# Kernel optimization log

Measured on AMD Instinct MI355X. Metric: run time of the kernel, lower is better.

## Reference

```python
import jax, jax.numpy as jnp
import numpy as np

B, V, D = 2048, 3129, 768  # batch, answer vocab, BERT embed dim


def setup_inputs() -> dict:
    key = jax.random.key(0)
    k1, k2, k3, k4 = jax.random.split(key, 4)
    prediction = jax.random.normal(k1, (B, V), dtype=jnp.float32)
    # sparse multi-label soft scores: ~10 nonzero answers per row (VQA-style)
    soft = jax.random.uniform(k2, (B, V), dtype=jnp.float32)
    keep = jax.random.uniform(k3, (B, V)) < 0.003
    label = jnp.where(keep, soft, 0.0)
    Embedding = jax.random.normal(k4, (V, D), dtype=jnp.float32)
    return {"prediction": prediction, "label": label, "Embedding": Embedding}


def reference(prediction, label, Embedding):
    V_ = Embedding.shape[0]
    # cosine-style normalization of the Gram matrix (row norms of sim itself,
    # exactly as in the torch code)
    sim = Embedding @ Embedding.T                              # [V, V]
    n = jnp.sqrt((sim ** 2).sum(1, keepdims=True))             # [V, 1]
    sim = sim / (n @ n.T + 1e-8)
    sim = jnp.where(jnp.eye(V_, dtype=bool), -2.0, sim)        # mask diagonal
    mapping = jnp.argmax(sim, axis=1)                          # [V] int

    # vectorized replacement of the per-batch/per-nonzero python loop:
    # semantic_a[i, mapping[g]] = label[i, g] for every nonzero label[i, g].
    # entries with label==0 are routed to out-of-bounds index V and dropped.
    Bn = label.shape[0]
    idx = jnp.where(label != 0, mapping[None, :], V_)          # [B, V]
    rows = jnp.arange(Bn)[:, None]                             # [B, 1]
    semantic_a = jnp.zeros_like(label).at[rows, idx].set(label, mode="drop")

    # BCE-with-logits, mean reduction, scaled by labels.size(1)
    bce = jnp.logaddexp(0.0, prediction) - prediction * semantic_a
    return jnp.mean(bce) * V_
```

## Files before the change

### kernel.cpp

```cpp
#include <hip/hip_runtime.h>
#include <hip/hip_bf16.h>

#define VN 3129
#define DN 768
#define BN 2048
#define NT 3200
#define NB64 50
#define NTRI64 1275

typedef __attribute__((ext_vector_type(8))) short bf16x8;
typedef __attribute__((ext_vector_type(4))) float f32x4;

typedef __attribute__((address_space(3))) void as3_void;
typedef __attribute__((address_space(1))) const void as1_cvoid;

__device__ __forceinline__ void gload16(const void* g, void* l) {
    __builtin_amdgcn_global_load_lds((as1_cvoid*)g, (as3_void*)l, 16, 0, 0);
}

__device__ __forceinline__ unsigned sortable_f32(float f) {
    unsigned u = __float_as_uint(f);
    return (u & 0x80000000u) ? ~u : (u | 0x80000000u);
}

static const size_t WB_EB  = 0;
static const size_t WB_N2  = 4915200;
static const size_t WB_ARG = 4928000;
static const size_t WB_P1  = 4940800;
static const size_t WB_P2  = 4948992;
static const size_t WB_GSL = 4957184;
static const size_t WB_LSL = 5481472;
static const size_t WB_CNT = 6005760;
static const size_t WS_NEEDED = 6013952;
static const int GRID_PREP = 2048;

__global__ __launch_bounds__(256) void k_prep(const float* __restrict__ E,
                                              const float* __restrict__ pred,
                                              const float* __restrict__ label,
                                              unsigned short* __restrict__ Eb,
                                              unsigned* __restrict__ zwords,
                                              float* __restrict__ part1,
                                              unsigned* __restrict__ gsl,
                                              float* __restrict__ lsl,
                                              unsigned* __restrict__ cntarr) {
    const int tid = threadIdx.x;
    const int gid = blockIdx.x * 256 + tid;
    const int gstride = gridDim.x * 256;
    const int lane = tid & 63;

    for (int i = gid; i < 6400; i += gstride) zwords[i] = 0u;

    const int nchunks = NT * DN / 8;
    for (int chunk = gid; chunk < nchunks; chunk += gstride) {
        int row = chunk / (DN / 8);
        int cc = (chunk % (DN / 8)) * 8;
        unsigned short o[8];
        if (row < VN) {
            const float* src = E + (size_t)row * DN + cc;
            float4 a = *(const float4*)src;
            float4 b = *(const float4*)(src + 4);
            float v[8] = {a.x, a.y, a.z, a.w, b.x, b.y, b.z, b.w};
#pragma unroll
            for (int t = 0; t < 8; ++t) {
                unsigned u = __float_as_uint(v[t]);
                u += 0x7FFFu + ((u >> 16) & 1u);
                o[t] = (unsigned short)(u >> 16);
            }
        } else {
#pragma unroll
            for (int t = 0; t < 8; ++t) o[t] = 0;
        }
        *(uint4*)(Eb + (size_t)chunk * 8) = *(const uint4*)o;
    }

    {
        const float4* p4 = (const float4*)pred;
        const int n4 = BN * VN / 4;
        float acc = 0.f;
        for (int i = gid; i < n4; i += gstride) {
            float4 v = p4[i];
            acc += fmaxf(v.x, 0.f) + __logf(1.f + __expf(-fabsf(v.x)));
            acc += fmaxf(v.y, 0.f) + __logf(1.f + __expf(-fabsf(v.y)));
            acc += fmaxf(v.z, 0.f) + __logf(1.f + __expf(-fabsf(v.z)));
            acc += fmaxf(v.w, 0.f) + __logf(1.f + __expf(-fabsf(v.w)));
        }
        for (int off = 32; off; off >>= 1) acc += __shfl_down(acc, off);
        __shared__ float wsum[4];
        int wid = tid >> 6;
        if (lane == 0) wsum[wid] = acc;
        __syncthreads();
        if (tid == 0) part1[blockIdx.x] = wsum[0] + wsum[1] + wsum[2] + wsum[3];
    }

    {
        const int wave_gid = gid >> 6;
        if (wave_gid < BN) {
            const int row = wave_gid;
            const float* lrow = label + (size_t)row * VN;
            float4 buf[12];
#pragma unroll
            for (int c = 0; c < 12; ++c)
                buf[c] = *(const float4*)(lrow + c * 256 + lane * 4);
            float tailv = 0.f;
            const int gtail = 3072 + lane;
            if (lane < VN - 3072) tailv = lrow[gtail];

            int base = 0;
#pragma unroll
            for (int c = 0; c < 12; ++c) {
                const float* f = (const float*)&buf[c];
#pragma unroll
                for (int e = 0; e < 4; ++e) {
                    float l = f[e];
                    unsigned long long mask = __ballot(l != 0.f);
                    if (l != 0.f) {
                        int pos = base + __popcll(mask & ((1ull << lane) - 1ull));
                        if (pos < 64) {
                            gsl[row * 64 + pos] = (unsigned)(c * 256 + lane * 4 + e);
                            lsl[row * 64 + pos] = l;
                        }
                    }
                    base += __popcll(mask);
                }
            }
            {
                unsigned long long mask = __ballot(tailv != 0.f);
                if (tailv != 0.f) {
                    int pos = base + __popcll(mask & ((1ull << lane) - 1ull));
                    if (pos < 64) {
                        gsl[row * 64 + pos] = (unsigned)gtail;
                        lsl[row * 64 + pos] = tailv;
                    }
                }
                base += __popcll(mask);
            }
            if (lane == 0) cntarr[row] = (unsigned)base;
        }
    }
}

template <int PASS>
__global__ __launch_bounds__(256) void k_gram64(const unsigned short* __restrict__ Eb,
                                                float* __restrict__ n2,
                                                unsigned* __restrict__ argbest) {
    __shared__ __align__(16) unsigned short As[64 * 64];
    __shared__ __align__(16) unsigned short Bs[64 * 64];
    const int tid = threadIdx.x;
    const int lane = tid & 63;
    const int w = tid >> 6;
    const int wr = w >> 1, wc = w & 1;

    int t = blockIdx.x, bi = 0, rem = t;
    while (rem >= NB64 - bi) { rem -= NB64 - bi; ++bi; }
    const int bj = bi + rem;
    const int i0 = bi * 64, j0 = bj * 64;

    const int srow = lane >> 3;
    const int scol = 8 * ((lane & 7) ^ (lane >> 3));

    f32x4 acc[2][2] = {};

    for (int k0 = 0; k0 < DN; k0 += 64) {
#pragma unroll
        for (int q = 0; q < 2; ++q) {
            int ci = w * 2 + q;
            int row = ci * 8 + srow;
            gload16(Eb + (size_t)(i0 + row) * DN + k0 + scol, As + ci * 512);
            gload16(Eb + (size_t)(j0 + row) * DN + k0 + scol, Bs + ci * 512);
        }
        __syncthreads();
        const int rA = wr * 32 + (lane & 15);
        const int rB = wc * 32 + (lane & 15);
        const int swr = (lane & 7) << 4;
        const int kb = (lane >> 4) * 16;
#pragma unroll
        for (int ks = 0; ks < 2; ++ks) {
            const int cb = (kb + ks * 64) ^ swr;
            bf16x8 af[2], bfr[2];
#pragma unroll
            for (int m = 0; m < 2; ++m)
                af[m] = *(const bf16x8*)((const char*)As + (rA + m * 16) * 128 + cb);
#pragma unroll
            for (int n = 0; n < 2; ++n)
                bfr[n] = *(const bf16x8*)((const char*)Bs + (rB + n * 16) * 128 + cb);
#pragma unroll
            for (int m = 0; m < 2; ++m)
#pragma unroll
                for (int n = 0; n < 2; ++n)
                    acc[m][n] = __builtin_amdgcn_mfma_f32_16x16x32_bf16(
                        af[m], bfr[n], acc[m][n], 0, 0, 0);
        }
        __syncthreads();
    }

    const int rr4 = (lane >> 4) * 4;

    if (PASS == 0) {
        __shared__ float red[64];
        if (tid < 64) red[tid] = 0.f;
        __syncthreads();
#pragma unroll
        for (int m = 0; m < 2; ++m)
#pragma unroll
            for (int i = 0; i < 4; ++i) {
                float s = acc[m][0][i] * acc[m][0][i] + acc[m][1][i] * acc[m][1][i];
                s += __shfl_xor(s, 1); s += __shfl_xor(s, 2);
                s += __shfl_xor(s, 4); s += __shfl_xor(s, 8);
                if ((lane & 15) == 0)
                    atomicAdd(&red[wr * 32 + m * 16 + rr4 + i], s);
            }
        __syncthreads();
        if (tid < 64) atomicAdd(&n2[i0 + tid], red[tid]);
        if (bi != bj) {
            __syncthreads();
            if (tid < 64) red[tid] = 0.f;
            __syncthreads();
#pragma unroll
            for (int n = 0; n < 2; ++n) {
                float s = 0.f;
#pragma unroll
                for (int m = 0; m < 2; ++m)
#pragma unroll
                    for (int i = 0; i < 4; ++i) { float x = acc[m][n][i]; s += x * x; }
                s += __shfl_xor(s, 16); s += __shfl_xor(s, 32);
                if (lane < 16)
                    atomicAdd(&red[wc * 32 + n * 16 + lane], s);
            }
            __syncthreads();
            if (tid < 64) atomicAdd(&n2[j0 + tid], red[tid]);
        }
    } else {
        __shared__ float rni_s[64], rnj_s[64];
        __shared__ unsigned rbest[64], cbest[64];
        if (tid < 64) {
            rni_s[tid] = rsqrtf(n2[i0 + tid]);
            rnj_s[tid] = rsqrtf(n2[j0 + tid]);
            rbest[tid] = 0u; cbest[tid] = 0u;
        }
        __syncthreads();

        int rg[8]; float rni8[8];
#pragma unroll
        for (int m = 0; m < 2; ++m)
#pragma unroll
            for (int i = 0; i < 4; ++i) {
                int rl = wr * 32 + m * 16 + rr4 + i;
                rg[m * 4 + i] = i0 + rl;
                rni8[m * 4 + i] = rni_s[rl];
            }
        int cg2[2]; float rnj2[2];
#pragma unroll
        for (int n = 0; n < 2; ++n) {
            int cl = wc * 32 + n * 16 + (lane & 15);
            cg2[n] = j0 + cl;
            rnj2[n] = rnj_s[cl];
        }

#pragma unroll
        for (int m = 0; m < 2; ++m)
#pragma unroll
            for (int i = 0; i < 4; ++i) {
                int ig = rg[m * 4 + i];
                unsigned best = 0u;
#pragma unroll
                for (int n = 0; n < 2; ++n) {
                    int jg = cg2[n];
                    if (jg < VN && jg != ig) {
                        unsigned key = (sortable_f32(acc[m][n][i] * rnj2[n]) & 0xFFFFF000u)
                                       | (unsigned)jg;
                        best = max(best, key);
                    }
                }
                best = max(best, __shfl_xor(best, 1));
                best = max(best, __shfl_xor(best, 2));
                best = max(best, __shfl_xor(best, 4));
                best = max(best, __shfl_xor(best, 8));
                if ((lane & 15) == 0)
                    atomicMax(&rbest[wr * 32 + m * 16 + rr4 + i], best);
            }

        if (bi != bj) {
#pragma unroll
            for (int n = 0; n < 2; ++n) {
                unsigned best = 0u;
#pragma unroll
                for (int m = 0; m < 2; ++m)
#pragma unroll
                    for (int i = 0; i < 4; ++i) {
                        int ig = rg[m * 4 + i];
                        if (ig < VN) {
                            unsigned key = (sortable_f32(acc[m][n][i] * rni8[m * 4 + i]) & 0xFFFFF000u)
                                           | (unsigned)ig;
                            best = max(best, key);
                        }
                    }
                best = max(best, __shfl_xor(best, 16));
                best = max(best, __shfl_xor(best, 32));
                if (lane < 16)
                    atomicMax(&cbest[wc * 32 + n * 16 + lane], best);
            }
        }
        __syncthreads();
        if (tid < 64) {
            unsigned rb = rbest[tid];
            if (rb) atomicMax(&argbest[i0 + tid], rb);
            if (bi != bj) {
                unsigned cb = cbest[tid];
                if (cb) atomicMax(&argbest[j0 + tid], cb);
            }
        }
    }
}

__global__ __launch_bounds__(64) void k_scatter(const float* __restrict__ pred,
                                                const float* __restrict__ label,
                                                const unsigned* __restrict__ argbest,
                                                const unsigned* __restrict__ gsl,
                                                const float* __restrict__ lsl,
                                                const unsigned* __restrict__ cntarr,
                                                float* __restrict__ part2) {
    const int i = blockIdx.x;
    const int lane = threadIdx.x;
    const int cnt = (int)cntarr[i];
    float contrib = 0.f;

    if (cnt <= 64) {
        unsigned g = 0, tgt = 0xFFFFFFFFu;
        float l = 0.f;
        if (lane < cnt) {
            g = gsl[i * 64 + lane];
            l = lsl[i * 64 + lane];
            tgt = argbest[g] & 0xFFFu;
        }
        __shared__ unsigned tg_s[64], g_s[64];
        tg_s[lane] = tgt; g_s[lane] = g;
        __syncthreads();
        if (lane < cnt) {
            bool keep = true;
            for (int o = 0; o < cnt; ++o)
                if (tg_s[o] == tgt && g_s[o] > g) { keep = false; break; }
            if (keep) contrib = pred[(size_t)i * VN + tgt] * l;
        }
    } else {
        __shared__ int c2;
        __shared__ unsigned short gs2[256], ts2[256];
        __shared__ float ls2[256];
        if (lane == 0) c2 = 0;
        __syncthreads();
        const float* lrow = label + (size_t)i * VN;
        for (int g = lane; g < VN; g += 64) {
            float l = lrow[g];
            if (l != 0.f) {
                int p = atomicAdd(&c2, 1);
                if (p < 256) {
                    gs2[p] = (unsigned short)g;
                    ls2[p] = l;
                    ts2[p] = (unsigned short)(argbest[g] & 0xFFFu);
                }
            }
        }
        __syncthreads();
        int m = min(c2, 256);
        for (int e = lane; e < m; e += 64) {
            bool keep = true;
            for (int o = 0; o < m; ++o)
                if (ts2[o] == ts2[e] && gs2[o] > gs2[e]) keep = false;
            if (keep) contrib += pred[(size_t)i * VN + ts2[e]] * ls2[e];
        }
    }

    for (int off = 32; off; off >>= 1) contrib += __shfl_down(contrib, off);
    if (lane == 0) part2[i] = contrib;
}

__global__ __launch_bounds__(256) void k_final(const float* __restrict__ part1, int p1n,
                                               const float* __restrict__ part2,
                                               float* __restrict__ out) {
    int tid = threadIdx.x;
    double acc = 0.0;
    for (int i = tid; i < p1n; i += 256) acc += (double)part1[i];
    for (int i = tid; i < BN; i += 256) acc -= (double)part2[i];
    __shared__ double red[256];
    red[tid] = acc;
    __syncthreads();
    for (int s = 128; s; s >>= 1) {
        if (tid < s) red[tid] += red[tid + s];
        __syncthreads();
    }
    if (tid == 0) out[0] = (float)(red[0] / (double)BN);
}

__global__ __launch_bounds__(256) void k_zero(unsigned int* p, int nwords) {
    int idx = blockIdx.x * 256 + threadIdx.x;
    for (int i = idx; i < nwords; i += gridDim.x * 256) p[i] = 0u;
}

__global__ __launch_bounds__(256) void k_logexp(const float* __restrict__ pred,
                                                float* __restrict__ part1) {
    int tid = threadIdx.x;
    const float4* p4 = (const float4*)pred;
    const int n4 = BN * VN / 4;
    float acc = 0.f;
    for (int i = blockIdx.x * 256 + tid; i < n4; i += gridDim.x * 256) {
        float4 v = p4[i];
        acc += fmaxf(v.x, 0.f) + log1pf(__expf(-fabsf(v.x)));
        acc += fmaxf(v.y, 0.f) + log1pf(__expf(-fabsf(v.y)));
        acc += fmaxf(v.z, 0.f) + log1pf(__expf(-fabsf(v.z)));
        acc += fmaxf(v.w, 0.f) + log1pf(__expf(-fabsf(v.w)));
    }
    for (int off = 32; off; off >>= 1) acc += __shfl_down(acc, off);
    __shared__ float wsum[4];
    int lane = tid & 63, wid = tid >> 6;
    if (lane == 0) wsum[wid] = acc;
    __syncthreads();
    if (tid == 0) part1[blockIdx.x] = wsum[0] + wsum[1] + wsum[2] + wsum[3];
}

template <int PASS>
__global__ __launch_bounds__(256) void k_gemm(const float* __restrict__ E,
                                              float* __restrict__ n2,
                                              unsigned* __restrict__ argbest) {
    __shared__ float As[16][132];
    __shared__ float Bs[16][132];
    const int tid = threadIdx.x;
    const int tx = tid & 15, ty = tid >> 4;
    const int i0 = blockIdx.y * 128, j0 = blockIdx.x * 128;
    float acc[8][8] = {};

    for (int k0 = 0; k0 < DN; k0 += 16) {
#pragma unroll
        for (int h = 0; h < 2; ++h) {
            int f = tid + h * 256;
            int r = f >> 2;
            int kq = (f & 3) << 2;
            int gi = i0 + r;
            float4 va = make_float4(0.f, 0.f, 0.f, 0.f);
            if (gi < VN) va = *(const float4*)(E + gi * DN + k0 + kq);
            As[kq + 0][r] = va.x; As[kq + 1][r] = va.y;
            As[kq + 2][r] = va.z; As[kq + 3][r] = va.w;
            int gj = j0 + r;
            float4 vb = make_float4(0.f, 0.f, 0.f, 0.f);
            if (gj < VN) vb = *(const float4*)(E + gj * DN + k0 + kq);
            Bs[kq + 0][r] = vb.x; Bs[kq + 1][r] = vb.y;
            Bs[kq + 2][r] = vb.z; Bs[kq + 3][r] = vb.w;
        }
        __syncthreads();
#pragma unroll
        for (int k = 0; k < 16; ++k) {
            float a[8], b[8];
            *(float4*)&a[0] = *(const float4*)&As[k][ty * 8];
            *(float4*)&a[4] = *(const float4*)&As[k][ty * 8 + 4];
            *(float4*)&b[0] = *(const float4*)&Bs[k][tx * 8];
            *(float4*)&b[4] = *(const float4*)&Bs[k][tx * 8 + 4];
#pragma unroll
            for (int m = 0; m < 8; ++m)
#pragma unroll
                for (int n = 0; n < 8; ++n)
                    acc[m][n] = fmaf(a[m], b[n], acc[m][n]);
        }
        __syncthreads();
    }

    if (PASS == 0) {
        __shared__ float nrow[128];
        if (tid < 128) nrow[tid] = 0.f;
        __syncthreads();
#pragma unroll
        for (int m = 0; m < 8; ++m) {
            float s = 0.f;
#pragma unroll
            for (int n = 0; n < 8; ++n) s += acc[m][n] * acc[m][n];
            atomicAdd(&nrow[ty * 8 + m], s);
        }
        __syncthreads();
        if (tid < 128 && i0 + tid < VN) atomicAdd(&n2[i0 + tid], nrow[tid]);
    } else {
        __shared__ unsigned brow[128];
        if (tid < 128) brow[tid] = 0u;
        __syncthreads();
        float rnj[8];
#pragma unroll
        for (int n = 0; n < 8; ++n) {
            int j = j0 + tx * 8 + n;
            rnj[n] = (j < VN) ? rsqrtf(n2[j]) : 0.f;
        }
#pragma unroll
        for (int m = 0; m < 8; ++m) {
            int i = i0 + ty * 8 + m;
            unsigned best = 0u;
#pragma unroll
            for (int n = 0; n < 8; ++n) {
                int j = j0 + tx * 8 + n;
                if (j < VN && j != i) {
                    unsigned key = (sortable_f32(acc[m][n] * rnj[n]) & 0xFFFFF000u) | (unsigned)j;
                    best = max(best, key);
                }
            }
            atomicMax(&brow[ty * 8 + m], best);
        }
        __syncthreads();
        if (tid < 128 && i0 + tid < VN) atomicMax(&argbest[i0 + tid], brow[tid]);
    }
}

__global__ __launch_bounds__(256) void k_scatter_scan(const float* __restrict__ pred,
                                                      const float* __restrict__ label,
                                                      const unsigned* __restrict__ argbest,
                                                      float* __restrict__ part2) {
    int i = blockIdx.x;
    int tid = threadIdx.x;
    __shared__ int cnt;
    __shared__ unsigned short gs[256];
    __shared__ unsigned short ts[256];
    __shared__ float ls[256];
    if (tid == 0) cnt = 0;
    __syncthreads();
    const float* lrow = label + (size_t)i * VN;
    for (int g = tid; g < VN; g += 256) {
        float l = lrow[g];
        if (l != 0.f) {
            int p = atomicAdd(&cnt, 1);
            if (p < 256) {
                gs[p] = (unsigned short)g;
                ls[p] = l;
                ts[p] = (unsigned short)(argbest[g] & 0xFFFu);
            }
        }
    }
    __syncthreads();
    int m = min(cnt, 256);
    float contrib = 0.f;
    for (int e = tid; e < m; e += 256) {
        bool keep = true;
        for (int o = 0; o < m; ++o)
            if (ts[o] == ts[e] && gs[o] > gs[e]) keep = false;
        if (keep) contrib += pred[(size_t)i * VN + ts[e]] * ls[e];
    }
    for (int off = 32; off; off >>= 1) contrib += __shfl_down(contrib, off);
    __shared__ float wsum[4];
    int lane = tid & 63, wid = tid >> 6;
    if (lane == 0) wsum[wid] = contrib;
    __syncthreads();
    if (tid == 0) part2[i] = wsum[0] + wsum[1] + wsum[2] + wsum[3];
}

extern "C" void kernel_launch(void* const* d_in, const int* in_sizes, int n_in,
                              void* d_out, int out_size, void* d_ws, size_t ws_size,
                              hipStream_t stream) {
    (void)in_sizes; (void)n_in; (void)out_size;
    const float* pred  = (const float*)d_in[0];
    const float* label = (const float*)d_in[1];
    const float* E     = (const float*)d_in[2];
    float* out = (float*)d_out;
    char* wsb = (char*)d_ws;

    if (ws_size >= WS_NEEDED) {
        unsigned short* Eb = (unsigned short*)(wsb + WB_EB);
        float* n2    = (float*)(wsb + WB_N2);
        unsigned* argbest = (unsigned*)(wsb + WB_ARG);
        float* part1 = (float*)(wsb + WB_P1);
        float* part2 = (float*)(wsb + WB_P2);
        unsigned* gsl = (unsigned*)(wsb + WB_GSL);
        float* lsl   = (float*)(wsb + WB_LSL);
        unsigned* cntarr = (unsigned*)(wsb + WB_CNT);

        k_prep<<<GRID_PREP, 256, 0, stream>>>(E, pred, label, Eb, (unsigned*)n2,
                                              part1, gsl, lsl, cntarr);
        k_gram64<0><<<NTRI64, 256, 0, stream>>>(Eb, n2, argbest);
        k_gram64<1><<<NTRI64, 256, 0, stream>>>(Eb, n2, argbest);
        k_scatter<<<BN, 64, 0, stream>>>(pred, label, argbest, gsl, lsl, cntarr, part2);
        k_final<<<1, 256, 0, stream>>>(part1, GRID_PREP, part2, out);
    } else {
        float* ws = (float*)d_ws;
        float* n2    = ws;
        unsigned* argbest = (unsigned*)(ws + 3200);
        float* part1 = ws + 6400;
        float* part2 = ws + 8448;
        k_zero<<<10, 256, 0, stream>>>((unsigned int*)ws, 6400);
        k_logexp<<<2048, 256, 0, stream>>>(pred, part1);
        dim3 g((VN + 127) / 128, (VN + 127) / 128);
        k_gemm<0><<<g, 256, 0, stream>>>(E, n2, argbest);
        k_gemm<1><<<g, 256, 0, stream>>>(E, n2, argbest);
        k_scatter_scan<<<BN, 256, 0, stream>>>(pred, label, argbest, part2);
        k_final<<<1, 256, 0, stream>>>(part1, 2048, part2, out);
    }
}
```

Baseline: 62.96 us.

## Store Gram tiles as bf16 once instead of recomputing GEMM for argmax pass

Before, the upper-triangular bf16 Gram GEMM ran twice, once to accumulate row norms and once to find the argmax. Now the first pass also writes each tile's accumulators to workspace as round-to-nearest bf16. A new lightweight kernel reloads those tiles, normalizes them and does the argmax without redoing the MFMA work. Both kernels also remap block IDs across XCDs for locality. The trade is extra global traffic (about 10 MB written and read) and extra workspace. Rounding similarities to bf16 before comparing could change argmax ties or near-ties.

```diff
diff --git a/kernel.cpp b/kernel.cpp
--- a/kernel.cpp
+++ b/kernel.cpp
@@ -23,15 +23,22 @@
     return (u & 0x80000000u) ? ~u : (u | 0x80000000u);
 }
 
+__device__ __forceinline__ int xcd_swz(int orig) {
+    const int q = NTRI64 / 8, r = NTRI64 % 8;
+    int xcd = orig & 7, idx = orig >> 3;
+    return (xcd < r ? xcd * (q + 1) : r * (q + 1) + (xcd - r) * q) + idx;
+}
+
 static const size_t WB_EB  = 0;
-static const size_t WB_N2  = 4915200;
-static const size_t WB_ARG = 4928000;
-static const size_t WB_P1  = 4940800;
-static const size_t WB_P2  = 4948992;
-static const size_t WB_GSL = 4957184;
-static const size_t WB_LSL = 5481472;
-static const size_t WB_CNT = 6005760;
-static const size_t WS_NEEDED = 6013952;
+static const size_t WB_SIM = 4915200;
+static const size_t WB_N2  = 15360000;
+static const size_t WB_ARG = 15372800;
+static const size_t WB_P1  = 15385600;
+static const size_t WB_P2  = 15393792;
+static const size_t WB_GSL = 15401984;
+static const size_t WB_LSL = 15926272;
+static const size_t WB_CNT = 16450560;
+static const size_t WS_NEEDED = 16458752;
 static const int GRID_PREP = 2048;
 
 __global__ __launch_bounds__(256) void k_prep(const float* __restrict__ E,
@@ -139,10 +146,9 @@
     }
 }
 
-template <int PASS>
-__global__ __launch_bounds__(256) void k_gram64(const unsigned short* __restrict__ Eb,
-                                                float* __restrict__ n2,
-                                                unsigned* __restrict__ argbest) {
+__global__ __launch_bounds__(256) void k_gram64s(const unsigned short* __restrict__ Eb,
+                                                 float* __restrict__ n2,
+                                                 unsigned short* __restrict__ simT) {
     __shared__ __align__(16) unsigned short As[64 * 64];
     __shared__ __align__(16) unsigned short Bs[64 * 64];
     const int tid = threadIdx.x;
@@ -150,7 +156,7 @@
     const int w = tid >> 6;
     const int wr = w >> 1, wc = w & 1;
 
-    int t = blockIdx.x, bi = 0, rem = t;
+    int t = xcd_swz(blockIdx.x), bi = 0, rem = t;
     while (rem >= NB64 - bi) { rem -= NB64 - bi; ++bi; }
     const int bj = bi + rem;
     const int i0 = bi * 64, j0 = bj * 64;
@@ -195,119 +201,156 @@
 
     const int rr4 = (lane >> 4) * 4;
 
-    if (PASS == 0) {
-        __shared__ float red[64];
+    {
+        unsigned op[8];
+#pragma unroll
+        for (int m = 0; m < 2; ++m)
+#pragma unroll
+            for (int n = 0; n < 2; ++n)
+#pragma unroll
+                for (int ih = 0; ih < 2; ++ih) {
+                    unsigned lo = __float_as_uint(acc[m][n][ih * 2]);
+                    lo += 0x7FFFu + ((lo >> 16) & 1u);
+                    unsigned hi = __float_as_uint(acc[m][n][ih * 2 + 1]);
+                    hi += 0x7FFFu + ((hi >> 16) & 1u);
+                    op[(m * 2 + n) * 2 + ih] = (lo >> 16) | (hi & 0xFFFF0000u);
+                }
+        uint4* dst = (uint4*)(simT + (size_t)t * 4096 + (size_t)tid * 16);
+        dst[0] = *(uint4*)&op[0];
+        dst[1] = *(uint4*)&op[4];
+    }
+
+    __shared__ float red[64];
+    if (tid < 64) red[tid] = 0.f;
+    __syncthreads();
+#pragma unroll
+    for (int m = 0; m < 2; ++m)
+#pragma unroll
+        for (int i = 0; i < 4; ++i) {
+            float s = acc[m][0][i] * acc[m][0][i] + acc[m][1][i] * acc[m][1][i];
+            s += __shfl_xor(s, 1); s += __shfl_xor(s, 2);
+            s += __shfl_xor(s, 4); s += __shfl_xor(s, 8);
+            if ((lane & 15) == 0)
+                atomicAdd(&red[wr * 32 + m * 16 + rr4 + i], s);
+        }
+    __syncthreads();
+    if (tid < 64) atomicAdd(&n2[i0 + tid], red[tid]);
+    if (bi != bj) {
+        __syncthreads();
         if (tid < 64) red[tid] = 0.f;
         __syncthreads();
 #pragma unroll
-        for (int m = 0; m < 2; ++m)
-#pragma unroll
-            for (int i = 0; i < 4; ++i) {
-                float s = acc[m][0][i] * acc[m][0][i] + acc[m][1][i] * acc[m][1][i];
-                s += __shfl_xor(s, 1); s += __shfl_xor(s, 2);
-                s += __shfl_xor(s, 4); s += __shfl_xor(s, 8);
-                if ((lane & 15) == 0)
-                    atomicAdd(&red[wr * 32 + m * 16 + rr4 + i], s);
+        for (int n = 0; n < 2; ++n) {
+            float s = 0.f;
+#pragma unroll
+            for (int m = 0; m < 2; ++m)
+#pragma unroll
+                for (int i = 0; i < 4; ++i) { float x = acc[m][n][i]; s += x * x; }
+            s += __shfl_xor(s, 16); s += __shfl_xor(s, 32);
+            if (lane < 16)
+                atomicAdd(&red[wc * 32 + n * 16 + lane], s);
+        }
+        __syncthreads();
+        if (tid < 64) atomicAdd(&n2[j0 + tid], red[tid]);
+    }
+}
+
+__global__ __launch_bounds__(256) void k_amax64(const unsigned short* __restrict__ simT,
+                                                const float* __restrict__ n2,
+                                                unsigned* __restrict__ argbest) {
+    const int tid = threadIdx.x, lane = tid & 63, w = tid >> 6;
+    const int wr = w >> 1, wc = w & 1;
+    int t = xcd_swz(blockIdx.x), bi = 0, rem = t;
+    while (rem >= NB64 - bi) { rem -= NB64 - bi; ++bi; }
+    const int bj = bi + rem;
+    const int i0 = bi * 64, j0 = bj * 64;
+
+    __shared__ float rni_s[64], rnj_s[64];
+    __shared__ unsigned rbest[64], cbest[64];
+    if (tid < 64) {
+        rni_s[tid] = rsqrtf(n2[i0 + tid]);
+        rnj_s[tid] = rsqrtf(n2[j0 + tid]);
+        rbest[tid] = 0u; cbest[tid] = 0u;
+    }
+    __syncthreads();
+
+    const uint4* src = (const uint4*)(simT + (size_t)t * 4096 + (size_t)tid * 16);
+    uint4 iv0 = src[0], iv1 = src[1];
+    unsigned ip[8];
+    *(uint4*)&ip[0] = iv0; *(uint4*)&ip[4] = iv1;
+
+    const int rr4 = (lane >> 4) * 4;
+    int rg[8]; float rni8[8];
+#pragma unroll
+    for (int m = 0; m < 2; ++m)
+#pragma unroll
+        for (int i = 0; i < 4; ++i) {
+            int rl = wr * 32 + m * 16 + rr4 + i;
+            rg[m * 4 + i] = i0 + rl;
+            rni8[m * 4 + i] = rni_s[rl];
+        }
+    int cg2[2]; float rnj2[2];
+#pragma unroll
+    for (int n = 0; n < 2; ++n) {
+        int cl = wc * 32 + n * 16 + (lane & 15);
+        cg2[n] = j0 + cl;
+        rnj2[n] = rnj_s[cl];
+    }
+
+#pragma unroll
+    for (int m = 0; m < 2; ++m)
+#pragma unroll
+        for (int i = 0; i < 4; ++i) {
+            int ig = rg[m * 4 + i];
+            unsigned best = 0u;
+#pragma unroll
+            for (int n = 0; n < 2; ++n) {
+                int jg = cg2[n];
+                if (jg < VN && jg != ig) {
+                    unsigned wv = ip[(m * 2 + n) * 2 + (i >> 1)];
+                    float v = __uint_as_float((i & 1) ? (wv & 0xFFFF0000u) : (wv << 16));
+                    unsigned key = (sortable_f32(v * rnj2[n]) & 0xFFFFF000u) | (unsigned)jg;
+                    best = max(best, key);
+                }
             }
-        __syncthreads();
-        if (tid < 64) atomicAdd(&n2[i0 + tid], red[tid]);
-        if (bi != bj) {
-            __syncthreads();
-            if (tid < 64) red[tid] = 0.f;
-            __syncthreads();
-#pragma unroll
-            for (int n = 0; n < 2; ++n) {
-                float s = 0.f;
-#pragma unroll
-                for (int m = 0; m < 2; ++m)
-#pragma unroll
-                    for (int i = 0; i < 4; ++i) { float x = acc[m][n][i]; s += x * x; }
-                s += __shfl_xor(s, 16); s += __shfl_xor(s, 32);
-                if (lane < 16)
-                    atomicAdd(&red[wc * 32 + n * 16 + lane], s);
-            }
-            __syncthreads();
-            if (tid < 64) atomicAdd(&n2[j0 + tid], red[tid]);
-        }
-    } else {
-        __shared__ float rni_s[64], rnj_s[64];
-        __shared__ unsigned rbest[64], cbest[64];
-        if (tid < 64) {
-            rni_s[tid] = rsqrtf(n2[i0 + tid]);
-            rnj_s[tid] = rsqrtf(n2[j0 + tid]);
-            rbest[tid] = 0u; cbest[tid] = 0u;
-        }
-        __syncthreads();
-
-        int rg[8]; float rni8[8];
-#pragma unroll
-        for (int m = 0; m < 2; ++m)
-#pragma unroll
-            for (int i = 0; i < 4; ++i) {
-                int rl = wr * 32 + m * 16 + rr4 + i;
-                rg[m * 4 + i] = i0 + rl;
-                rni8[m * 4 + i] = rni_s[rl];
-            }
-        int cg2[2]; float rnj2[2];
+            best = max(best, __shfl_xor(best, 1));
+            best = max(best, __shfl_xor(best, 2));
+            best = max(best, __shfl_xor(best, 4));
+            best = max(best, __shfl_xor(best, 8));
+            if ((lane & 15) == 0)
+                atomicMax(&rbest[wr * 32 + m * 16 + rr4 + i], best);
+        }
+
+    if (bi != bj) {
 #pragma unroll
         for (int n = 0; n < 2; ++n) {
-            int cl = wc * 32 + n * 16 + (lane & 15);
-            cg2[n] = j0 + cl;
-            rnj2[n] = rnj_s[cl];
-        }
-
-#pragma unroll
-        for (int m = 0; m < 2; ++m)
-#pragma unroll
-            for (int i = 0; i < 4; ++i) {
-                int ig = rg[m * 4 + i];
-                unsigned best = 0u;
-#pragma unroll
-                for (int n = 0; n < 2; ++n) {
-                    int jg = cg2[n];
-                    if (jg < VN && jg != ig) {
-                        unsigned key = (sortable_f32(acc[m][n][i] * rnj2[n]) & 0xFFFFF000u)
-                                       | (unsigned)jg;
+            unsigned best = 0u;
+#pragma unroll
+            for (int m = 0; m < 2; ++m)
+#pragma unroll
+                for (int i = 0; i < 4; ++i) {
+                    int ig = rg[m * 4 + i];
+                    if (ig < VN) {
+                        unsigned wv = ip[(m * 2 + n) * 2 + (i >> 1)];
+                        float v = __uint_as_float((i & 1) ? (wv & 0xFFFF0000u) : (wv << 16));
+                        unsigned key = (sortable_f32(v * rni8[m * 4 + i]) & 0xFFFFF000u)
+                                       | (unsigned)ig;
                         best = max(best, key);
                     }
                 }
-                best = max(best, __shfl_xor(best, 1));
-                best = max(best, __shfl_xor(best, 2));
-                best = max(best, __shfl_xor(best, 4));
-                best = max(best, __shfl_xor(best, 8));
-                if ((lane & 15) == 0)
-                    atomicMax(&rbest[wr * 32 + m * 16 + rr4 + i], best);
-            }
-
+            best = max(best, __shfl_xor(best, 16));
+            best = max(best, __shfl_xor(best, 32));
+            if (lane < 16)
+                atomicMax(&cbest[wc * 32 + n * 16 + lane], best);
+        }
+    }
+    __syncthreads();
+    if (tid < 64) {
+        unsigned rb = rbest[tid];
+        if (rb) atomicMax(&argbest[i0 + tid], rb);
         if (bi != bj) {
-#pragma unroll
-            for (int n = 0; n < 2; ++n) {
-                unsigned best = 0u;
-#pragma unroll
-                for (int m = 0; m < 2; ++m)
-#pragma unroll
-                    for (int i = 0; i < 4; ++i) {
-                        int ig = rg[m * 4 + i];
-                        if (ig < VN) {
-                            unsigned key = (sortable_f32(acc[m][n][i] * rni8[m * 4 + i]) & 0xFFFFF000u)
-                                           | (unsigned)ig;
-                            best = max(best, key);
-                        }
-                    }
-                best = max(best, __shfl_xor(best, 16));
-                best = max(best, __shfl_xor(best, 32));
-                if (lane < 16)
-                    atomicMax(&cbest[wc * 32 + n * 16 + lane], best);
-            }
-        }
-        __syncthreads();
-        if (tid < 64) {
-            unsigned rb = rbest[tid];
-            if (rb) atomicMax(&argbest[i0 + tid], rb);
-            if (bi != bj) {
-                unsigned cb = cbest[tid];
-                if (cb) atomicMax(&argbest[j0 + tid], cb);
-            }
+            unsigned cb = cbest[tid];
+            if (cb) atomicMax(&argbest[j0 + tid], cb);
         }
     }
 }
@@ -555,7 +598,8 @@
     char* wsb = (char*)d_ws;
 
     if (ws_size >= WS_NEEDED) {
-        unsigned short* Eb = (unsigned short*)(wsb + WB_EB);
+        unsigned short* Eb   = (unsigned short*)(wsb + WB_EB);
+        unsigned short* simT = (unsigned short*)(wsb + WB_SIM);
         float* n2    = (float*)(wsb + WB_N2);
         unsigned* argbest = (unsigned*)(wsb + WB_ARG);
         float* part1 = (float*)(wsb + WB_P1);
@@ -566,8 +610,8 @@
 
         k_prep<<<GRID_PREP, 256, 0, stream>>>(E, pred, label, Eb, (unsigned*)n2,
                                               part1, gsl, lsl, cntarr);
-        k_gram64<0><<<NTRI64, 256, 0, stream>>>(Eb, n2, argbest);
-        k_gram64<1><<<NTRI64, 256, 0, stream>>>(Eb, n2, argbest);
+        k_gram64s<<<NTRI64, 256, 0, stream>>>(Eb, n2, simT);
+        k_amax64<<<NTRI64, 256, 0, stream>>>(simT, n2, argbest);
         k_scatter<<<BN, 64, 0, stream>>>(pred, label, argbest, gsl, lsl, cntarr, part2);
         k_final<<<1, 256, 0, stream>>>(part1, GRID_PREP, part2, out);
     } else {
```

Result: faster. 54.38 us (-13.6%).
